# Kernel tuning notes

Measured on AMD Instinct MI355X. Metric: run time of the kernel, lower is better.

## Reference

```python
import jax, jax.numpy as jnp
import numpy as np

WS = 8
NUM_HEADS = 8
BLUR_STRENGTH = 1.0
EPS = 1e-5


def setup_inputs() -> dict:
    key = jax.random.key(0)
    ks = jax.random.split(key, 8)
    B, C, H, W = 8, 256, 128, 128
    FF = 1024
    inp = {
        'x': jax.random.normal(ks[0], (B, C, H, W), jnp.float32),
        'blur_map': jax.random.uniform(ks[1], (B, 1, H // 4, W // 4), jnp.float32),
        'qkv_w': jax.random.normal(ks[2], (C, 3 * C), jnp.float32) * 0.02,
        'qkv_b': jnp.zeros((3 * C,), jnp.float32),
        'proj_w': jax.random.normal(ks[3], (C, C), jnp.float32) * 0.02,
        'proj_b': jnp.zeros((C,), jnp.float32),
        'ff1_w': jax.random.normal(ks[4], (C, FF), jnp.float32) * 0.02,
        'ff1_b': jnp.zeros((FF,), jnp.float32),
        'ff2_w': jax.random.normal(ks[5], (FF, C), jnp.float32) * 0.02,
        'ff2_b': jnp.zeros((C,), jnp.float32),
        'n1_g': jnp.ones((C,), jnp.float32),
        'n1_b': jnp.zeros((C,), jnp.float32),
        'n2_g': jnp.ones((C,), jnp.float32),
        'n2_b': jnp.zeros((C,), jnp.float32),
    }
    return inp


def _layer_norm(y, g, b):
    mu = jnp.mean(y, axis=-1, keepdims=True)
    var = jnp.mean(jnp.square(y - mu), axis=-1, keepdims=True)
    return (y - mu) * jax.lax.rsqrt(var + EPS) * g + b


def reference(x, blur_map, qkv_w, qkv_b, proj_w, proj_b, ff1_w, ff1_b, ff2_w, ff2_b, n1_g, n1_b, n2_g, n2_b):
    B, C, H, W = x.shape
    ws = WS
    h = NUM_HEADS
    hd = C // h
    T = ws * ws
    scale = C ** (-0.5)  # note: full dim, matching the torch module

    # window partition -> [nw, T, C]
    xw = x.reshape(B, C, H // ws, ws, W // ws, ws)
    xw = xw.transpose(0, 2, 4, 3, 5, 1).reshape(-1, T, C)
    nw = xw.shape[0]

    qkv = (xw @ qkv_w + qkv_b).reshape(nw, T, 3, h, hd).transpose(2, 0, 3, 1, 4)
    q, k, v = qkv[0], qkv[1], qkv[2]  # [nw, h, T, hd]

    attn = jnp.einsum('whid,whjd->whij', q, k) * scale

    # blur modulation along the key axis
    blur_down = jax.image.resize(blur_map, (B, 1, H, W), 'bilinear')
    blur_w = blur_down.reshape(B, 1, H // ws, ws, W // ws, ws)
    blur_w = blur_w.transpose(0, 2, 4, 3, 5, 1).reshape(nw, T)
    attn = attn * (1.0 + BLUR_STRENGTH * blur_w)[:, None, None, :]

    attn = jax.nn.softmax(attn, axis=-1)
    out = jnp.einsum('whij,whjd->whid', attn, v)
    out = out.transpose(0, 2, 1, 3).reshape(nw, T, C)
    out = out @ proj_w + proj_b

    x1 = xw + _layer_norm(out, n1_g, n1_b)
    ff = jnp.maximum(x1 @ ff1_w + ff1_b, 0.0) @ ff2_w + ff2_b
    x2 = x1 + _layer_norm(ff, n2_g, n2_b)

    # window reverse -> [B, C, H, W]
    x2 = x2.reshape(B, H // ws, W // ws, ws, ws, C)
    return x2.transpose(0, 5, 1, 3, 2, 4).reshape(B, C, H, W)
```

## Files before the change

kernel.cpp:

```cpp
#include <hip/hip_runtime.h>
#include <hip/hip_bf16.h>
#include <cstdint>

typedef _Float16 half8 __attribute__((ext_vector_type(8)));
typedef _Float16 half4 __attribute__((ext_vector_type(4)));
typedef float f32x4 __attribute__((ext_vector_type(4)));

__device__ __forceinline__ void gload_lds16(const _Float16* g, _Float16* l) {
  __builtin_amdgcn_global_load_lds(
      (const __attribute__((address_space(1))) void*)g,
      (__attribute__((address_space(3))) void*)l, 16, 0, 0);
}

__global__ __launch_bounds__(256) void wtrans(const float* __restrict__ W,
                                              _Float16* __restrict__ WT, int K, int N) {
  int idx = blockIdx.x * 256 + threadIdx.x;
  if (idx >= K * N) return;
  int k = idx / N, n = idx - k * N;
  WT[(size_t)n * K + k] = (_Float16)W[idx];
}

__global__ __launch_bounds__(256) void blur_prep(const float* __restrict__ bm,
                                                 float* __restrict__ bw) {
  int idx = blockIdx.x * 256 + threadIdx.x;
  int wi = idx >> 6, t = idx & 63;
  int b = wi >> 8, wid = wi & 255;
  int hw = wid >> 4, ww = wid & 15;
  int hh = hw * 8 + (t >> 3), www = ww * 8 + (t & 7);
  float yf = (hh + 0.5f) * 0.25f - 0.5f;
  float xf = (www + 0.5f) * 0.25f - 0.5f;
  float yfl = floorf(yf), xfl = floorf(xf);
  float fy = yf - yfl, fx = xf - xfl;
  int y0 = (int)yfl, x0 = (int)xfl;
  int y1 = y0 + 1, x1 = x0 + 1;
  if (y0 < 0) y0 = 0; if (x0 < 0) x0 = 0;
  if (y1 > 31) y1 = 31; if (x1 > 31) x1 = 31;
  const float* p = bm + (size_t)b * 1024;
  float v00 = p[y0 * 32 + x0], v01 = p[y0 * 32 + x1];
  float v10 = p[y1 * 32 + x0], v11 = p[y1 * 32 + x1];
  float v0 = v00 + fx * (v01 - v00);
  float v1 = v10 + fx * (v11 - v10);
  bw[idx] = v0 + fy * (v1 - v0);
}

__global__ __launch_bounds__(256) void gather_x(const float* __restrict__ x,
                                                _Float16* __restrict__ xw) {
  const int c0 = blockIdx.x << 6;
  const int hh = blockIdx.y;
  const int b  = blockIdx.z;
  __shared__ float tile[64][133];
  const int tid = threadIdx.x;
  {
    const int cl = tid >> 7, p = tid & 127;
    const float* xp = x + ((size_t)(b * 256 + c0) * 128 + hh) * 128 + p;
#pragma unroll
    for (int i = 0; i < 32; ++i) {
      int c = i * 2 + cl;
      tile[c][p] = xp[(size_t)c * 16384];
    }
  }
  __syncthreads();
  const int w = tid >> 6, lane = tid & 63;
  const int hw = hh >> 3, ts = hh & 7;
#pragma unroll
  for (int i = 0; i < 32; ++i) {
    int pp = i * 4 + w;
    int row = ((b * 256 + hw * 16 + (pp >> 3)) << 6) + ts * 8 + (pp & 7);
    xw[(size_t)row * 256 + c0 + lane] = (_Float16)tile[lane][pp];
  }
}

__global__ __launch_bounds__(256) void scatter_out(const _Float16* __restrict__ x2,
                                                   float* __restrict__ out) {
  const int c0 = blockIdx.x << 6;
  const int hh = blockIdx.y;
  const int b  = blockIdx.z;
  __shared__ float tile[64][133];
  const int tid = threadIdx.x;
  const int w = tid >> 6, lane = tid & 63;
  const int hw = hh >> 3, ts = hh & 7;
#pragma unroll
  for (int i = 0; i < 32; ++i) {
    int pp = i * 4 + w;
    int row = ((b * 256 + hw * 16 + (pp >> 3)) << 6) + ts * 8 + (pp & 7);
    tile[lane][pp] = (float)x2[(size_t)row * 256 + c0 + lane];
  }
  __syncthreads();
  const int cl = tid >> 7, p = tid & 127;
  float* op = out + ((size_t)(b * 256 + c0) * 128 + hh) * 128 + p;
#pragma unroll
  for (int i = 0; i < 32; ++i) {
    int c = i * 2 + cl;
    op[(size_t)c * 16384] = tile[c][p];
  }
}

template<int RELU>
__global__ __launch_bounds__(256) void gemm_f16(const _Float16* __restrict__ A,
    const _Float16* __restrict__ BT, const float* __restrict__ bias,
    _Float16* __restrict__ C, int M, int N, int K) {
  __shared__ _Float16 As[128 * 32];
  __shared__ _Float16 Bs[128 * 32];
  const int tid = threadIdx.x;
  const int m0 = blockIdx.y << 7;
  const int n0 = blockIdx.x << 7;
  const int w = tid >> 6, lane = tid & 63;
  const int wr = (w >> 1) << 6, wc = (w & 1) << 6;
  const int lr = lane & 15, lg = lane >> 4;
  f32x4 acc[4][4] = {};
  const int sr = tid >> 2, skk = (tid & 3) << 3;
  const _Float16* Ag = A + (size_t)(m0 + sr) * K + skk;
  const _Float16* Bg = BT + (size_t)(n0 + sr) * K + skk;
  const size_t halfstep = (size_t)64 * K;
  for (int k0 = 0; k0 < K; k0 += 32) {
    __syncthreads();
    gload_lds16(Ag + k0,            &As[(size_t)tid * 8]);
    gload_lds16(Ag + k0 + halfstep, &As[(size_t)(256 + tid) * 8]);
    gload_lds16(Bg + k0,            &Bs[(size_t)tid * 8]);
    gload_lds16(Bg + k0 + halfstep, &Bs[(size_t)(256 + tid) * 8]);
    __syncthreads();
    half8 af[4], bf[4];
#pragma unroll
    for (int t = 0; t < 4; ++t)
      af[t] = *(const half8*)&As[(wr + t * 16 + lr) * 32 + lg * 8];
#pragma unroll
    for (int t = 0; t < 4; ++t)
      bf[t] = *(const half8*)&Bs[(wc + t * 16 + lr) * 32 + lg * 8];
#pragma unroll
    for (int i = 0; i < 4; ++i)
#pragma unroll
      for (int j = 0; j < 4; ++j)
        acc[i][j] = __builtin_amdgcn_mfma_f32_16x16x32_f16(af[i], bf[j], acc[i][j], 0, 0, 0);
  }
  float bv[4];
#pragma unroll
  for (int j = 0; j < 4; ++j) bv[j] = bias[n0 + wc + j * 16 + lr];
#pragma unroll
  for (int i = 0; i < 4; ++i) {
#pragma unroll
    for (int j = 0; j < 4; ++j) {
      int row = m0 + wr + i * 16 + lg * 4;
      int col = n0 + wc + j * 16 + lr;
      _Float16* cp = C + (size_t)row * N + col;
#pragma unroll
      for (int rr = 0; rr < 4; ++rr) {
        float v = acc[i][j][rr] + bv[j];
        if (RELU) v = fmaxf(v, 0.0f);
        cp[(size_t)rr * N] = (_Float16)v;
      }
    }
  }
}

#define ATT_SWZ(row, col) (((row) << 6) + ((col) ^ (((row) & 7) << 3)))
__global__ __launch_bounds__(256, 3) void attn_mfma(const _Float16* __restrict__ qkv,
    const float* __restrict__ bw, _Float16* __restrict__ o) {
  const int wdw = blockIdx.x;
  const int w = threadIdx.x >> 6;
  const int lane = threadIdx.x & 63;
  const int lr = lane & 15, lg = lane >> 4;
  __shared__ _Float16 lds_p[4][64 * 64];
  __shared__ _Float16 lds_v[4][32 * 64];
  _Float16* Pb = lds_p[w];
  _Float16* Vt = lds_v[w];
  const size_t base = (size_t)wdw * 49152;
  f32x4 blv[4];
#pragma unroll
  for (int jt = 0; jt < 4; ++jt) {
    f32x4 bv = *(const f32x4*)&bw[wdw * 64 + jt * 16 + lg * 4];
    blv[jt] = bv * 0.0625f + 0.0625f;
  }
  const f32x4 zero4 = {0.f, 0.f, 0.f, 0.f};
#pragma unroll
  for (int hi = 0; hi < 2; ++hi) {
    const int h = w + hi * 4;
    const size_t qo = base + (size_t)h * 32;
    const _Float16* kp = qkv + qo + 256 + (size_t)lr * 768 + lg * 8;
    const _Float16* qp = qkv + qo +       (size_t)lr * 768 + lg * 8;
    half8 ak[4], bq[4];
#pragma unroll
    for (int t = 0; t < 4; ++t) {
      ak[t] = *(const half8*)(kp + (size_t)t * 16 * 768);
      bq[t] = *(const half8*)(qp + (size_t)t * 16 * 768);
    }
    const _Float16* vp = qkv + qo + 512 + (size_t)lane * 768;
#pragma unroll
    for (int e = 0; e < 4; ++e) {
      half8 vv = *(const half8*)(vp + e * 8);
#pragma unroll
      for (int d = 0; d < 8; ++d) Vt[ATT_SWZ(e * 8 + d, lane)] = vv[d];
    }
    f32x4 cst[4][4];
#pragma unroll
    for (int jt = 0; jt < 4; ++jt)
#pragma unroll
      for (int it = 0; it < 4; ++it)
        cst[jt][it] = __builtin_amdgcn_mfma_f32_16x16x32_f16(ak[jt], bq[it], zero4, 0, 0, 0);
#pragma unroll
    for (int it = 0; it < 4; ++it) {
      float m = -1e30f;
#pragma unroll
      for (int jt = 0; jt < 4; ++jt) {
        cst[jt][it] *= blv[jt];
        m = fmaxf(m, fmaxf(fmaxf(cst[jt][it][0], cst[jt][it][1]),
                           fmaxf(cst[jt][it][2], cst[jt][it][3])));
      }
      m = fmaxf(m, __shfl_xor(m, 16, 64));
      m = fmaxf(m, __shfl_xor(m, 32, 64));
      float s = 0.f;
#pragma unroll
      for (int jt = 0; jt < 4; ++jt)
#pragma unroll
        for (int r = 0; r < 4; ++r) {
          float e = __expf(cst[jt][it][r] - m);
          cst[jt][it][r] = e;
          s += e;
        }
      s += __shfl_xor(s, 16, 64);
      s += __shfl_xor(s, 32, 64);
      float inv = 1.0f / s;
#pragma unroll
      for (int jt = 0; jt < 4; ++jt) {
        half4 pv;
#pragma unroll
        for (int r = 0; r < 4; ++r) pv[r] = (_Float16)(cst[jt][it][r] * inv);
        *(half4*)&Pb[ATT_SWZ(it * 16 + lr, jt * 16 + lg * 4)] = pv;
      }
    }
    f32x4 co[4][2] = {};
#pragma unroll
    for (int ks = 0; ks < 2; ++ks) {
      half8 bv2[2], pa[4];
#pragma unroll
      for (int dt = 0; dt < 2; ++dt)
        bv2[dt] = *(const half8*)&Vt[ATT_SWZ(dt * 16 + lr, ks * 32 + lg * 8)];
#pragma unroll
      for (int it = 0; it < 4; ++it)
        pa[it] = *(const half8*)&Pb[ATT_SWZ(it * 16 + lr, ks * 32 + lg * 8)];
#pragma unroll
      for (int it = 0; it < 4; ++it)
#pragma unroll
        for (int dt = 0; dt < 2; ++dt)
          co[it][dt] = __builtin_amdgcn_mfma_f32_16x16x32_f16(pa[it], bv2[dt], co[it][dt], 0, 0, 0);
    }
#pragma unroll
    for (int it = 0; it < 4; ++it)
#pragma unroll
      for (int dt = 0; dt < 2; ++dt)
#pragma unroll
        for (int r = 0; r < 4; ++r) {
          int row = it * 16 + lg * 4 + r;
          o[((size_t)wdw * 64 + row) * 256 + h * 32 + dt * 16 + lr] =
              (_Float16)co[it][dt][r];
        }
  }
}

__global__ __launch_bounds__(256) void ln_add(const _Float16* __restrict__ inp,
    const _Float16* __restrict__ res, const float* __restrict__ gg,
    const float* __restrict__ bb, _Float16* __restrict__ out) {
  const int w = threadIdx.x >> 6, lane = threadIdx.x & 63;
  const size_t row = (size_t)blockIdx.x * 4 + w;
  half4 v = ((const half4*)(inp + row * 256))[lane];
  float f0 = (float)v[0], f1 = (float)v[1], f2 = (float)v[2], f3 = (float)v[3];
  float s = f0 + f1 + f2 + f3;
  float s2 = f0*f0 + f1*f1 + f2*f2 + f3*f3;
#pragma unroll
  for (int m = 1; m < 64; m <<= 1) {
    s  += __shfl_xor(s, m, 64);
    s2 += __shfl_xor(s2, m, 64);
  }
  float mu = s * 0.00390625f;
  float var = s2 * 0.00390625f - mu * mu;
  float rs = rsqrtf(var + 1e-5f);
  f32x4 gv = *(const f32x4*)(gg + lane * 4);
  f32x4 bv = *(const f32x4*)(bb + lane * 4);
  half4 rv = ((const half4*)(res + row * 256))[lane];
  half4 ov;
  ov[0] = (_Float16)((f0 - mu) * rs * gv[0] + bv[0] + (float)rv[0]);
  ov[1] = (_Float16)((f1 - mu) * rs * gv[1] + bv[1] + (float)rv[1]);
  ov[2] = (_Float16)((f2 - mu) * rs * gv[2] + bv[2] + (float)rv[2]);
  ov[3] = (_Float16)((f3 - mu) * rs * gv[3] + bv[3] + (float)rv[3]);
  ((half4*)(out + row * 256))[lane] = ov;
}

__global__ __launch_bounds__(256) void sentinel(float* out, int n) {
  int i = blockIdx.x * 256 + threadIdx.x;
  if (i < n) out[i] = 12345.0f;
}

extern "C" void kernel_launch(void* const* d_in, const int* in_sizes, int n_in,
                              void* d_out, int out_size, void* d_ws, size_t ws_size,
                              hipStream_t stream) {
  const float* x      = (const float*)d_in[0];
  const float* blurm  = (const float*)d_in[1];
  const float* qkv_w  = (const float*)d_in[2];
  const float* qkv_b  = (const float*)d_in[3];
  const float* proj_w = (const float*)d_in[4];
  const float* proj_b = (const float*)d_in[5];
  const float* ff1_w  = (const float*)d_in[6];
  const float* ff1_b  = (const float*)d_in[7];
  const float* ff2_w  = (const float*)d_in[8];
  const float* ff2_b  = (const float*)d_in[9];
  const float* n1_g   = (const float*)d_in[10];
  const float* n1_b   = (const float*)d_in[11];
  const float* n2_g   = (const float*)d_in[12];
  const float* n2_b   = (const float*)d_in[13];
  float* out = (float*)d_out;

  char* ws = (char*)d_ws;
  constexpr size_t OFF_RA  = 0;
  constexpr size_t OFF_XW  = 201326592ull;
  constexpr size_t OFF_AO  = OFF_XW + 67108864ull;
  constexpr size_t OFF_RC  = OFF_AO + 67108864ull;
  constexpr size_t OFF_X1  = OFF_RC + 67108864ull;
  constexpr size_t OFF_QW  = OFF_X1 + 67108864ull;
  constexpr size_t OFF_PW  = OFF_QW + 393216ull;
  constexpr size_t OFF_F1W = OFF_PW + 131072ull;
  constexpr size_t OFF_F2W = OFF_F1W + 524288ull;
  constexpr size_t OFF_BL  = OFF_F2W + 524288ull;
  constexpr size_t NEED    = OFF_BL + 524288ull;
  if (ws_size < NEED) {
    sentinel<<<(out_size + 255) / 256, 256, 0, stream>>>(out, out_size);
    return;
  }
  _Float16* RA   = (_Float16*)(ws + OFF_RA);
  _Float16* xw_h = (_Float16*)(ws + OFF_XW);
  _Float16* ao   = (_Float16*)(ws + OFF_AO);
  _Float16* rc   = (_Float16*)(ws + OFF_RC);
  _Float16* x1h  = (_Float16*)(ws + OFF_X1);
  _Float16* qwT  = (_Float16*)(ws + OFF_QW);
  _Float16* pwT  = (_Float16*)(ws + OFF_PW);
  _Float16* f1wT = (_Float16*)(ws + OFF_F1W);
  _Float16* f2wT = (_Float16*)(ws + OFF_F2W);
  float* blurw   = (float*)(ws + OFF_BL);

  wtrans<<<768, 256, 0, stream>>>(qkv_w, qwT, 256, 768);
  wtrans<<<256, 256, 0, stream>>>(proj_w, pwT, 256, 256);
  wtrans<<<1024, 256, 0, stream>>>(ff1_w, f1wT, 256, 1024);
  wtrans<<<1024, 256, 0, stream>>>(ff2_w, f2wT, 1024, 256);
  blur_prep<<<512, 256, 0, stream>>>(blurm, blurw);
  gather_x<<<dim3(4, 128, 8), 256, 0, stream>>>(x, xw_h);

  gemm_f16<0><<<dim3(6, 1024), 256, 0, stream>>>(xw_h, qwT, qkv_b, RA, 131072, 768, 256);
  attn_mfma<<<2048, 256, 0, stream>>>(RA, blurw, ao);
  gemm_f16<0><<<dim3(2, 1024), 256, 0, stream>>>(ao, pwT, proj_b, rc, 131072, 256, 256);
  ln_add<<<32768, 256, 0, stream>>>(rc, xw_h, n1_g, n1_b, x1h);
  for (int ch = 0; ch < 2; ++ch) {
    gemm_f16<1><<<dim3(8, 512), 256, 0, stream>>>(x1h + (size_t)ch * 65536 * 256, f1wT, ff1_b,
                                                  RA, 65536, 1024, 256);
    gemm_f16<0><<<dim3(2, 512), 256, 0, stream>>>(RA, f2wT, ff2_b,
                                                  rc + (size_t)ch * 65536 * 256, 65536, 256, 1024);
  }
  ln_add<<<32768, 256, 0, stream>>>(rc, x1h, n2_g, n2_b, xw_h);
  scatter_out<<<dim3(4, 128, 8), 256, 0, stream>>>(xw_h, out);
}
```

Measured before the change: 654.4 us.

## Fuse layernorm-residual into full-width GEMM epilogue; swizzle LDS and remap workgroups

Adds a gemm_ln kernel that computes a 128x256 output tile per block, so a whole 256-wide row is resident and the bias, layernorm and residual add run in the epilogue. It replaces the proj and ff2 GEMMs plus both ln_add passes, removing the intermediate fp16 round trip through global memory and two kernel launches. It also XOR-swizzles the LDS k-offsets in both GEMMs to reduce bank conflicts and remaps block indices across groups of eight for cache/XCD locality. The fused kernel uses twice the accumulators and a larger B tile, which may lower occupancy.

```diff
diff --git a/kernel.cpp b/kernel.cpp
--- a/kernel.cpp
+++ b/kernel.cpp
@@ -11,6 +11,8 @@
       (const __attribute__((address_space(1))) void*)g,
       (__attribute__((address_space(3))) void*)l, 16, 0, 0);
 }
+
+#define KSWZ(r) ((((r) >> 1) & 3) << 3)
 
 __global__ __launch_bounds__(256) void wtrans(const float* __restrict__ W,
                                               _Float16* __restrict__ WT, int K, int N) {
@@ -102,13 +104,17 @@
   __shared__ _Float16 As[128 * 32];
   __shared__ _Float16 Bs[128 * 32];
   const int tid = threadIdx.x;
-  const int m0 = blockIdx.y << 7;
-  const int n0 = blockIdx.x << 7;
+  const int gx = gridDim.x;
+  int flat = blockIdx.y * gx + blockIdx.x;
+  int nwg = gx * gridDim.y;
+  int nb = (nwg & 7) ? flat : ((flat & 7) * (nwg >> 3) + (flat >> 3));
+  const int m0 = (nb / gx) << 7;
+  const int n0 = (nb % gx) << 7;
   const int w = tid >> 6, lane = tid & 63;
   const int wr = (w >> 1) << 6, wc = (w & 1) << 6;
   const int lr = lane & 15, lg = lane >> 4;
   f32x4 acc[4][4] = {};
-  const int sr = tid >> 2, skk = (tid & 3) << 3;
+  const int sr = tid >> 2, skk = ((tid & 3) << 3) ^ KSWZ(tid >> 2);
   const _Float16* Ag = A + (size_t)(m0 + sr) * K + skk;
   const _Float16* Bg = BT + (size_t)(n0 + sr) * K + skk;
   const size_t halfstep = (size_t)64 * K;
@@ -121,11 +127,15 @@
     __syncthreads();
     half8 af[4], bf[4];
 #pragma unroll
-    for (int t = 0; t < 4; ++t)
-      af[t] = *(const half8*)&As[(wr + t * 16 + lr) * 32 + lg * 8];
-#pragma unroll
-    for (int t = 0; t < 4; ++t)
-      bf[t] = *(const half8*)&Bs[(wc + t * 16 + lr) * 32 + lg * 8];
+    for (int t = 0; t < 4; ++t) {
+      int rowA = wr + t * 16 + lr;
+      af[t] = *(const half8*)&As[rowA * 32 + ((lg * 8) ^ KSWZ(rowA))];
+    }
+#pragma unroll
+    for (int t = 0; t < 4; ++t) {
+      int rowB = wc + t * 16 + lr;
+      bf[t] = *(const half8*)&Bs[rowB * 32 + ((lg * 8) ^ KSWZ(rowB))];
+    }
 #pragma unroll
     for (int i = 0; i < 4; ++i)
 #pragma unroll
@@ -150,6 +160,105 @@
       }
     }
   }
+}
+
+__global__ __launch_bounds__(256) void gemm_ln(const _Float16* __restrict__ A,
+    const _Float16* __restrict__ BT, const float* __restrict__ bias,
+    const _Float16* __restrict__ resid, const float* __restrict__ gg,
+    const float* __restrict__ bb, _Float16* __restrict__ out, int M, int K) {
+  __shared__ _Float16 As[128 * 32];
+  __shared__ _Float16 Bs[256 * 32];
+  __shared__ float part[128][2][2];
+  const int tid = threadIdx.x;
+  int flat = blockIdx.x;
+  int nwg = gridDim.x;
+  int nb = (nwg & 7) ? flat : ((flat & 7) * (nwg >> 3) + (flat >> 3));
+  const int m0 = nb << 7;
+  const int w = tid >> 6, lane = tid & 63;
+  const int wr = (w >> 1) << 6;
+  const int wc = (w & 1) << 7;
+  const int lr = lane & 15, lg = lane >> 4;
+  f32x4 acc[4][8] = {};
+  const int sr = tid >> 2, skk = ((tid & 3) << 3) ^ KSWZ(tid >> 2);
+  const _Float16* Ag = A + (size_t)(m0 + sr) * K + skk;
+  const _Float16* Bg = BT + (size_t)sr * K + skk;
+  const size_t step64 = (size_t)64 * K;
+  for (int k0 = 0; k0 < K; k0 += 32) {
+    __syncthreads();
+    gload_lds16(Ag + k0,              &As[(size_t)tid * 8]);
+    gload_lds16(Ag + k0 + step64,     &As[(size_t)(256 + tid) * 8]);
+    gload_lds16(Bg + k0,              &Bs[(size_t)tid * 8]);
+    gload_lds16(Bg + k0 + step64,     &Bs[(size_t)(256 + tid) * 8]);
+    gload_lds16(Bg + k0 + 2 * step64, &Bs[(size_t)(512 + tid) * 8]);
+    gload_lds16(Bg + k0 + 3 * step64, &Bs[(size_t)(768 + tid) * 8]);
+    __syncthreads();
+    half8 af[4], bf[8];
+#pragma unroll
+    for (int t = 0; t < 4; ++t) {
+      int rowA = wr + t * 16 + lr;
+      af[t] = *(const half8*)&As[rowA * 32 + ((lg * 8) ^ KSWZ(rowA))];
+    }
+#pragma unroll
+    for (int t = 0; t < 8; ++t) {
+      int rowB = wc + t * 16 + lr;
+      bf[t] = *(const half8*)&Bs[rowB * 32 + ((lg * 8) ^ KSWZ(rowB))];
+    }
+#pragma unroll
+    for (int i = 0; i < 4; ++i)
+#pragma unroll
+      for (int j = 0; j < 8; ++j)
+        acc[i][j] = __builtin_amdgcn_mfma_f32_16x16x32_f16(af[i], bf[j], acc[i][j], 0, 0, 0);
+  }
+  float biasv[8], gvv[8], bvv[8];
+#pragma unroll
+  for (int jt = 0; jt < 8; ++jt) {
+    int col = wc + jt * 16 + lr;
+    biasv[jt] = bias[col]; gvv[jt] = gg[col]; bvv[jt] = bb[col];
+  }
+#pragma unroll
+  for (int it = 0; it < 4; ++it)
+#pragma unroll
+    for (int jt = 0; jt < 8; ++jt) acc[it][jt] += biasv[jt];
+#pragma unroll
+  for (int it = 0; it < 4; ++it)
+#pragma unroll
+    for (int rr = 0; rr < 4; ++rr) {
+      float s = 0.f, s2 = 0.f;
+#pragma unroll
+      for (int jt = 0; jt < 8; ++jt) {
+        float v = acc[it][jt][rr];
+        s += v; s2 += v * v;
+      }
+#pragma unroll
+      for (int mk = 1; mk < 16; mk <<= 1) {
+        s  += __shfl_xor(s, mk, 64);
+        s2 += __shfl_xor(s2, mk, 64);
+      }
+      if (lr == 0) {
+        int rl = wr + it * 16 + lg * 4 + rr;
+        part[rl][w & 1][0] = s;
+        part[rl][w & 1][1] = s2;
+      }
+    }
+  __syncthreads();
+#pragma unroll
+  for (int it = 0; it < 4; ++it)
+#pragma unroll
+    for (int rr = 0; rr < 4; ++rr) {
+      int rl = wr + it * 16 + lg * 4 + rr;
+      float s  = part[rl][0][0] + part[rl][1][0];
+      float s2 = part[rl][0][1] + part[rl][1][1];
+      float mu = s * 0.00390625f;
+      float rs = rsqrtf(s2 * 0.00390625f - mu * mu + 1e-5f);
+      size_t row = (size_t)(m0 + rl);
+#pragma unroll
+      for (int jt = 0; jt < 8; ++jt) {
+        int col = wc + jt * 16 + lr;
+        float v = (acc[it][jt][rr] - mu) * rs * gvv[jt] + bvv[jt]
+                  + (float)resid[row * 256 + col];
+        out[row * 256 + col] = (_Float16)v;
+      }
+    }
 }
 
 #define ATT_SWZ(row, col) (((row) << 6) + ((col) ^ (((row) & 7) << 3)))
@@ -254,34 +363,6 @@
               (_Float16)co[it][dt][r];
         }
   }
-}
-
-__global__ __launch_bounds__(256) void ln_add(const _Float16* __restrict__ inp,
-    const _Float16* __restrict__ res, const float* __restrict__ gg,
-    const float* __restrict__ bb, _Float16* __restrict__ out) {
-  const int w = threadIdx.x >> 6, lane = threadIdx.x & 63;
-  const size_t row = (size_t)blockIdx.x * 4 + w;
-  half4 v = ((const half4*)(inp + row * 256))[lane];
-  float f0 = (float)v[0], f1 = (float)v[1], f2 = (float)v[2], f3 = (float)v[3];
-  float s = f0 + f1 + f2 + f3;
-  float s2 = f0*f0 + f1*f1 + f2*f2 + f3*f3;
-#pragma unroll
-  for (int m = 1; m < 64; m <<= 1) {
-    s  += __shfl_xor(s, m, 64);
-    s2 += __shfl_xor(s2, m, 64);
-  }
-  float mu = s * 0.00390625f;
-  float var = s2 * 0.00390625f - mu * mu;
-  float rs = rsqrtf(var + 1e-5f);
-  f32x4 gv = *(const f32x4*)(gg + lane * 4);
-  f32x4 bv = *(const f32x4*)(bb + lane * 4);
-  half4 rv = ((const half4*)(res + row * 256))[lane];
-  half4 ov;
-  ov[0] = (_Float16)((f0 - mu) * rs * gv[0] + bv[0] + (float)rv[0]);
-  ov[1] = (_Float16)((f1 - mu) * rs * gv[1] + bv[1] + (float)rv[1]);
-  ov[2] = (_Float16)((f2 - mu) * rs * gv[2] + bv[2] + (float)rv[2]);
-  ov[3] = (_Float16)((f3 - mu) * rs * gv[3] + bv[3] + (float)rv[3]);
-  ((half4*)(out + row * 256))[lane] = ov;
 }
 
 __global__ __launch_bounds__(256) void sentinel(float* out, int n) {
@@ -327,7 +408,6 @@
   _Float16* RA   = (_Float16*)(ws + OFF_RA);
   _Float16* xw_h = (_Float16*)(ws + OFF_XW);
   _Float16* ao   = (_Float16*)(ws + OFF_AO);
-  _Float16* rc   = (_Float16*)(ws + OFF_RC);
   _Float16* x1h  = (_Float16*)(ws + OFF_X1);
   _Float16* qwT  = (_Float16*)(ws + OFF_QW);
   _Float16* pwT  = (_Float16*)(ws + OFF_PW);
@@ -344,14 +424,13 @@
 
   gemm_f16<0><<<dim3(6, 1024), 256, 0, stream>>>(xw_h, qwT, qkv_b, RA, 131072, 768, 256);
   attn_mfma<<<2048, 256, 0, stream>>>(RA, blurw, ao);
-  gemm_f16<0><<<dim3(2, 1024), 256, 0, stream>>>(ao, pwT, proj_b, rc, 131072, 256, 256);
-  ln_add<<<32768, 256, 0, stream>>>(rc, xw_h, n1_g, n1_b, x1h);
+  gemm_ln<<<1024, 256, 0, stream>>>(ao, pwT, proj_b, xw_h, n1_g, n1_b, x1h, 131072, 256);
   for (int ch = 0; ch < 2; ++ch) {
-    gemm_f16<1><<<dim3(8, 512), 256, 0, stream>>>(x1h + (size_t)ch * 65536 * 256, f1wT, ff1_b,
+    const size_t off = (size_t)ch * 65536 * 256;
+    gemm_f16<1><<<dim3(8, 512), 256, 0, stream>>>(x1h + off, f1wT, ff1_b,
                                                   RA, 65536, 1024, 256);
-    gemm_f16<0><<<dim3(2, 512), 256, 0, stream>>>(RA, f2wT, ff2_b,
-                                                  rc + (size_t)ch * 65536 * 256, 65536, 256, 1024);
-  }
-  ln_add<<<32768, 256, 0, stream>>>(rc, x1h, n2_g, n2_b, xw_h);
+    gemm_ln<<<512, 256, 0, stream>>>(RA, f2wT, ff2_b, x1h + off, n2_g, n2_b,
+                                     xw_h + off, 65536, 1024);
+  }
   scatter_out<<<dim3(4, 128, 8), 256, 0, stream>>>(xw_h, out);
 }
```

New measurement: 710.9 us. 1.09x slower.
